# Performance work log

Hardware: AMD Instinct MI355X
Metric: run time of the kernel (lower is better)

Reference implementation:

```python
import jax, jax.numpy as jnp
import numpy as np

N = 4  # hypercomplex dimension

def setup_inputs() -> dict:
    key = jax.random.key(0)
    k1, k2, k3 = jax.random.split(key, 3)
    x = jax.random.normal(k1, (32, 196, 768), dtype=jnp.float32)
    # [n, out_pad/n, in_pad/n] = [4, 3072//4, 768//4]
    weight_components = jax.random.normal(k2, (N, 768, 192), dtype=jnp.float32) * 0.02
    bias = jax.random.normal(k3, (3072,), dtype=jnp.float32) * 0.02
    return {"x": x, "weight_components": weight_components, "bias": bias}

def reference(x, weight_components, bias):
    n, out_blk, in_blk = weight_components.shape
    batch_shape = x.shape[:-1]
    xb = x.reshape(-1, n, in_blk)  # [B, n, in_blk]
    # original: out[:, (i+j)%n] += x[:, j] @ W[i].T
    # equivalently out[:, k] = sum_j x[:, j] @ W[(k-j)%n].T
    k_idx = jnp.arange(n)[:, None]
    j_idx = jnp.arange(n)[None, :]
    Wperm = weight_components[(k_idx - j_idx) % n]  # [n(k), n(j), out_blk, in_blk]
    out = jnp.einsum('bjc,kjoc->bko', xb, Wperm)    # [B, n, out_blk]
    out = out.reshape(-1, n * out_blk) + bias
    return out.reshape(*batch_shape, n * out_blk)
```

## Files before the change

### kernel.cpp

```cpp
#include <hip/hip_runtime.h>
#include <stdint.h>

#define M_ROWS 6272
#define K_DIM  768
#define N_DIM  3072
#define BM 128
#define BN 128
#define BK 32

typedef unsigned short u16;
typedef __attribute__((ext_vector_type(8))) __bf16 bf16x8;
typedef __attribute__((ext_vector_type(4))) float f32x4;

__device__ __forceinline__ u16 f32_to_bf16(float f) {
    unsigned u = __float_as_uint(f);
    unsigned r = 0x7FFFu + ((u >> 16) & 1u);
    return (u16)((u + r) >> 16);
}

__device__ __forceinline__ unsigned pack2(float a, float b) {
    return (unsigned)f32_to_bf16(a) | ((unsigned)f32_to_bf16(b) << 16);
}

__global__ void cast_x_kernel(const float* __restrict__ x, u16* __restrict__ xb) {
    int idx = blockIdx.x * 256 + threadIdx.x;
    const float4* xp = (const float4*)x + (size_t)idx * 2;
    float4 a = xp[0], b = xp[1];
    uint4 v;
    v.x = pack2(a.x, a.y);
    v.y = pack2(a.z, a.w);
    v.z = pack2(b.x, b.y);
    v.w = pack2(b.z, b.w);
    ((uint4*)xb)[idx] = v;
}

__global__ void expand_w_kernel(const float* __restrict__ w, u16* __restrict__ wb) {
    int idx = blockIdx.x * 256 + threadIdx.x;
    int n    = idx / 96;
    int kc   = idx - n * 96;
    int kblk = n / 768;
    int o    = n - kblk * 768;
    int j    = kc / 24;
    int c8   = kc - j * 24;
    int i    = (kblk - j) & 3;
    const float* src = w + (((size_t)i * 768 + o) * 192 + c8 * 8);
    float4 a = ((const float4*)src)[0];
    float4 b = ((const float4*)src)[1];
    uint4 v;
    v.x = pack2(a.x, a.y);
    v.y = pack2(a.z, a.w);
    v.z = pack2(b.x, b.y);
    v.w = pack2(b.z, b.w);
    ((uint4*)wb)[idx] = v;
}

__device__ __forceinline__ void load_lds16(const u16* g, u16* l) {
    __builtin_amdgcn_global_load_lds(
        (const __attribute__((address_space(1))) void*)g,
        (__attribute__((address_space(3))) void*)l, 16, 0, 0);
}

__global__ __launch_bounds__(256) void gemm_bt(
    const u16* __restrict__ A,
    const u16* __restrict__ B,
    const float* __restrict__ bias,
    float* __restrict__ C)
{
    __shared__ u16 As[BM * BK];
    __shared__ u16 Bs[BN * BK];

    const int tid    = threadIdx.x;
    const int wave   = tid >> 6;
    const int lane   = tid & 63;
    const int lane16 = lane & 15;
    const int quad   = lane >> 4;
    const int wr     = wave >> 1;
    const int wc     = wave & 1;

    const int rowBase = blockIdx.y * BM;
    const int colBase = blockIdx.x * BN;

    const int c0 = tid;
    const int c1 = tid + 256;
    const u16* Ag0 = A + (size_t)(rowBase + (c0 >> 2)) * K_DIM + (c0 & 3) * 8;
    const u16* Ag1 = A + (size_t)(rowBase + (c1 >> 2)) * K_DIM + (c1 & 3) * 8;
    const u16* Bg0 = B + (size_t)(colBase + (c0 >> 2)) * K_DIM + (c0 & 3) * 8;
    const u16* Bg1 = B + (size_t)(colBase + (c1 >> 2)) * K_DIM + (c1 & 3) * 8;
    u16* Al0 = &As[c0 * 8];
    u16* Al1 = &As[c1 * 8];
    u16* Bl0 = &Bs[c0 * 8];
    u16* Bl1 = &Bs[c1 * 8];

    f32x4 acc[4][4] = {};

    for (int k0 = 0; k0 < K_DIM; k0 += BK) {
        __syncthreads();
        load_lds16(Ag0 + k0, Al0);
        load_lds16(Ag1 + k0, Al1);
        load_lds16(Bg0 + k0, Bl0);
        load_lds16(Bg1 + k0, Bl1);
        __syncthreads();

        bf16x8 af[4], bfv[4];
#pragma unroll
        for (int i = 0; i < 4; ++i)
            af[i] = *(const bf16x8*)&As[(wr * 64 + i * 16 + lane16) * BK + quad * 8];
#pragma unroll
        for (int j = 0; j < 4; ++j)
            bfv[j] = *(const bf16x8*)&Bs[(wc * 64 + j * 16 + lane16) * BK + quad * 8];
#pragma unroll
        for (int i = 0; i < 4; ++i)
#pragma unroll
            for (int j = 0; j < 4; ++j)
                acc[i][j] = __builtin_amdgcn_mfma_f32_16x16x32_bf16(
                    af[i], bfv[j], acc[i][j], 0, 0, 0);
    }

    float bv[4];
#pragma unroll
    for (int j = 0; j < 4; ++j)
        bv[j] = bias[colBase + wc * 64 + j * 16 + lane16];
#pragma unroll
    for (int i = 0; i < 4; ++i) {
        int row0 = rowBase + wr * 64 + i * 16 + quad * 4;
#pragma unroll
        for (int r = 0; r < 4; ++r) {
            float* cp = C + (size_t)(row0 + r) * N_DIM + colBase + wc * 64 + lane16;
#pragma unroll
            for (int j = 0; j < 4; ++j)
                cp[j * 16] = acc[i][j][r] + bv[j];
        }
    }
}

extern "C" void kernel_launch(void* const* d_in, const int* in_sizes, int n_in,
                              void* d_out, int out_size, void* d_ws, size_t ws_size,
                              hipStream_t stream) {
    const float* x    = (const float*)d_in[0];
    const float* w    = (const float*)d_in[1];
    const float* bias = (const float*)d_in[2];
    float* out = (float*)d_out;

    u16* xb = (u16*)d_ws;
    u16* wb = (u16*)((char*)d_ws + (size_t)M_ROWS * K_DIM * 2);

    hipLaunchKernelGGL(cast_x_kernel, dim3((M_ROWS * K_DIM / 8) / 256), dim3(256),
                       0, stream, x, xb);
    hipLaunchKernelGGL(expand_w_kernel, dim3((N_DIM * K_DIM / 8) / 256), dim3(256),
                       0, stream, w, wb);
    hipLaunchKernelGGL(gemm_bt, dim3(N_DIM / BN, M_ROWS / BM), dim3(256),
                       0, stream, xb, wb, bias, out);
}
```

Before: 138.9 us.

## Double-buffer LDS tiles with XOR swizzle and merge prep kernels

```diff
diff --git a/kernel.cpp b/kernel.cpp
--- a/kernel.cpp
+++ b/kernel.cpp
@@ -7,6 +7,12 @@
 #define BM 128
 #define BN 128
 #define BK 32
+#define NITER (K_DIM / BK)
+
+#define X_CHUNKS (M_ROWS * K_DIM / 8)
+#define W_CHUNKS (N_DIM * K_DIM / 8)
+#define X_BLOCKS (X_CHUNKS / 256)
+#define W_BLOCKS (W_CHUNKS / 256)
 
 typedef unsigned short u16;
 typedef __attribute__((ext_vector_type(8))) __bf16 bf16x8;
@@ -22,36 +28,38 @@
     return (unsigned)f32_to_bf16(a) | ((unsigned)f32_to_bf16(b) << 16);
 }
 
-__global__ void cast_x_kernel(const float* __restrict__ x, u16* __restrict__ xb) {
-    int idx = blockIdx.x * 256 + threadIdx.x;
-    const float4* xp = (const float4*)x + (size_t)idx * 2;
-    float4 a = xp[0], b = xp[1];
-    uint4 v;
-    v.x = pack2(a.x, a.y);
-    v.y = pack2(a.z, a.w);
-    v.z = pack2(b.x, b.y);
-    v.w = pack2(b.z, b.w);
-    ((uint4*)xb)[idx] = v;
-}
-
-__global__ void expand_w_kernel(const float* __restrict__ w, u16* __restrict__ wb) {
-    int idx = blockIdx.x * 256 + threadIdx.x;
-    int n    = idx / 96;
-    int kc   = idx - n * 96;
-    int kblk = n / 768;
-    int o    = n - kblk * 768;
-    int j    = kc / 24;
-    int c8   = kc - j * 24;
-    int i    = (kblk - j) & 3;
-    const float* src = w + (((size_t)i * 768 + o) * 192 + c8 * 8);
-    float4 a = ((const float4*)src)[0];
-    float4 b = ((const float4*)src)[1];
-    uint4 v;
-    v.x = pack2(a.x, a.y);
-    v.y = pack2(a.z, a.w);
-    v.z = pack2(b.x, b.y);
-    v.w = pack2(b.z, b.w);
-    ((uint4*)wb)[idx] = v;
+__global__ void prep_kernel(const float* __restrict__ x, const float* __restrict__ w,
+                            u16* __restrict__ xb, u16* __restrict__ wb) {
+    int b = blockIdx.x;
+    if (b < X_BLOCKS) {
+        int idx = b * 256 + threadIdx.x;
+        const float4* xp = (const float4*)x + (size_t)idx * 2;
+        float4 a = xp[0], c = xp[1];
+        uint4 v;
+        v.x = pack2(a.x, a.y);
+        v.y = pack2(a.z, a.w);
+        v.z = pack2(c.x, c.y);
+        v.w = pack2(c.z, c.w);
+        ((uint4*)xb)[idx] = v;
+    } else {
+        int idx = (b - X_BLOCKS) * 256 + threadIdx.x;
+        int n    = idx / 96;
+        int kc   = idx - n * 96;
+        int kblk = n / 768;
+        int o    = n - kblk * 768;
+        int j    = kc / 24;
+        int c8   = kc - j * 24;
+        int i    = (kblk - j) & 3;
+        const float* src = w + (((size_t)i * 768 + o) * 192 + c8 * 8);
+        float4 a = ((const float4*)src)[0];
+        float4 c = ((const float4*)src)[1];
+        uint4 v;
+        v.x = pack2(a.x, a.y);
+        v.y = pack2(a.z, a.w);
+        v.z = pack2(c.x, c.y);
+        v.w = pack2(c.z, c.w);
+        ((uint4*)wb)[idx] = v;
+    }
 }
 
 __device__ __forceinline__ void load_lds16(const u16* g, u16* l) {
@@ -66,8 +74,8 @@
     const float* __restrict__ bias,
     float* __restrict__ C)
 {
-    __shared__ u16 As[BM * BK];
-    __shared__ u16 Bs[BN * BK];
+    __shared__ u16 As[2][BM * BK];
+    __shared__ u16 Bs[2][BN * BK];
 
     const int tid    = threadIdx.x;
     const int wave   = tid >> 6;
@@ -82,32 +90,51 @@
 
     const int c0 = tid;
     const int c1 = tid + 256;
-    const u16* Ag0 = A + (size_t)(rowBase + (c0 >> 2)) * K_DIM + (c0 & 3) * 8;
-    const u16* Ag1 = A + (size_t)(rowBase + (c1 >> 2)) * K_DIM + (c1 & 3) * 8;
-    const u16* Bg0 = B + (size_t)(colBase + (c0 >> 2)) * K_DIM + (c0 & 3) * 8;
-    const u16* Bg1 = B + (size_t)(colBase + (c1 >> 2)) * K_DIM + (c1 & 3) * 8;
-    u16* Al0 = &As[c0 * 8];
-    u16* Al1 = &As[c1 * 8];
-    u16* Bl0 = &Bs[c0 * 8];
-    u16* Bl1 = &Bs[c1 * 8];
+    const int r0 = c0 >> 2, s0 = (c0 & 3) ^ ((r0 >> 1) & 3);
+    const int r1 = c1 >> 2, s1 = (c1 & 3) ^ ((r1 >> 1) & 3);
+    const u16* Ag0 = A + (size_t)(rowBase + r0) * K_DIM + s0 * 8;
+    const u16* Ag1 = A + (size_t)(rowBase + r1) * K_DIM + s1 * 8;
+    const u16* Bg0 = B + (size_t)(colBase + r0) * K_DIM + s0 * 8;
+    const u16* Bg1 = B + (size_t)(colBase + r1) * K_DIM + s1 * 8;
+    const int l0 = c0 * 8;
+    const int l1 = c1 * 8;
+
+    const int swz  = (lane16 >> 1) & 3;
+    const int slot = (quad ^ swz) * 8;
+    int aoff[4], boff[4];
+#pragma unroll
+    for (int i = 0; i < 4; ++i)
+        aoff[i] = (wr * 64 + i * 16 + lane16) * BK + slot;
+#pragma unroll
+    for (int j = 0; j < 4; ++j)
+        boff[j] = (wc * 64 + j * 16 + lane16) * BK + slot;
 
     f32x4 acc[4][4] = {};
 
-    for (int k0 = 0; k0 < K_DIM; k0 += BK) {
+    load_lds16(Ag0, &As[0][l0]);
+    load_lds16(Ag1, &As[0][l1]);
+    load_lds16(Bg0, &Bs[0][l0]);
+    load_lds16(Bg1, &Bs[0][l1]);
+
+#pragma unroll 2
+    for (int it = 0; it < NITER; ++it) {
+        const int cur = it & 1, nxt = cur ^ 1;
         __syncthreads();
-        load_lds16(Ag0 + k0, Al0);
-        load_lds16(Ag1 + k0, Al1);
-        load_lds16(Bg0 + k0, Bl0);
-        load_lds16(Bg1 + k0, Bl1);
-        __syncthreads();
+        if (it + 1 < NITER) {
+            const int k = (it + 1) * BK;
+            load_lds16(Ag0 + k, &As[nxt][l0]);
+            load_lds16(Ag1 + k, &As[nxt][l1]);
+            load_lds16(Bg0 + k, &Bs[nxt][l0]);
+            load_lds16(Bg1 + k, &Bs[nxt][l1]);
+        }
 
         bf16x8 af[4], bfv[4];
 #pragma unroll
         for (int i = 0; i < 4; ++i)
-            af[i] = *(const bf16x8*)&As[(wr * 64 + i * 16 + lane16) * BK + quad * 8];
+            af[i] = *(const bf16x8*)&As[cur][aoff[i]];
 #pragma unroll
         for (int j = 0; j < 4; ++j)
-            bfv[j] = *(const bf16x8*)&Bs[(wc * 64 + j * 16 + lane16) * BK + quad * 8];
+            bfv[j] = *(const bf16x8*)&Bs[cur][boff[j]];
 #pragma unroll
         for (int i = 0; i < 4; ++i)
 #pragma unroll
@@ -144,10 +171,8 @@
     u16* xb = (u16*)d_ws;
     u16* wb = (u16*)((char*)d_ws + (size_t)M_ROWS * K_DIM * 2);
 
-    hipLaunchKernelGGL(cast_x_kernel, dim3((M_ROWS * K_DIM / 8) / 256), dim3(256),
-                       0, stream, x, xb);
-    hipLaunchKernelGGL(expand_w_kernel, dim3((N_DIM * K_DIM / 8) / 256), dim3(256),
-                       0, stream, w, wb);
+    hipLaunchKernelGGL(prep_kernel, dim3(X_BLOCKS + W_BLOCKS), dim3(256),
+                       0, stream, x, w, xb, wb);
     hipLaunchKernelGGL(gemm_bt, dim3(N_DIM / BN, M_ROWS / BM), dim3(256),
                        0, stream, xb, wb, bias, out);
 }
```

Measured after the change: 140.0 us. No clear change (+0.8%).
